# Kernel optimization log

Hardware: AMD Instinct MI355X
Metric: run time of the kernel (lower is better)

The kernel has to match this reference:

```python
import jax, jax.numpy as jnp
import numpy as np

R_TOKEN_MAX = 32
R_CHAIN_MAX = 2
C_PAIR = 128
D_TOK = 2 * R_TOKEN_MAX + 2   # 66, one-hot depth for pos / token offsets
D_CHAIN = 2 * R_CHAIN_MAX + 2 # 6, one-hot depth for chain offsets
D_IN = 2 * D_TOK + 1 + D_CHAIN  # 139, Linear in_features


def setup_inputs() -> dict:
    key = jax.random.key(0)
    ks = jax.random.split(key, 6)
    B, N = 1, 1024
    residue_index = jnp.sort(jax.random.randint(ks[0], (B, N), 0, 1200, dtype=jnp.int32), axis=-1)
    token_index = jnp.broadcast_to(jnp.arange(N, dtype=jnp.int32), (B, N))
    asym_id = jnp.sort(jax.random.randint(ks[1], (B, N), 0, 8, dtype=jnp.int32), axis=-1)
    entity_id = jnp.sort(jax.random.randint(ks[2], (B, N), 0, 4, dtype=jnp.int32), axis=-1)
    sym_id = jax.random.randint(ks[3], (B, N), 0, 8, dtype=jnp.int32)
    W = jax.random.normal(ks[4], (D_IN, C_PAIR), dtype=jnp.float32) * 0.02
    return {
        'residue_index': residue_index,
        'token_index': token_index,
        'asym_id': asym_id,
        'entity_id': entity_id,
        'sym_id': sym_id,
        'W': W,
    }


def _offset_index(fi, r_max, is_same):
    # offset[i, j] = fi[i] - fi[j]  (torch: unsqueeze(-1) - unsqueeze(-2))
    off = fi[..., :, None] - fi[..., None, :]
    clipped = jnp.clip(off + r_max, 0, 2 * r_max)
    # pairs not satisfying is_same go to the sentinel bucket 2*r_max + 1
    return jnp.where(is_same, clipped, 2 * r_max + 1)


def reference(residue_index, token_index, asym_id, entity_id, sym_id, W):
    same_chain = asym_id[..., :, None] == asym_id[..., None, :]
    same_residue = residue_index[..., :, None] == residue_index[..., None, :]
    same_entity = entity_id[..., :, None] == entity_id[..., None, :]

    idx_pos = _offset_index(residue_index, R_TOKEN_MAX, same_residue)
    idx_tok = _offset_index(token_index, R_TOKEN_MAX, same_residue & same_chain)
    idx_chain = _offset_index(sym_id, R_CHAIN_MAX, ~same_chain)

    # Bias-free Linear on concatenated one-hots == sum of gathered weight rows.
    Wp = W[:D_TOK]                    # rel_pos block
    Wt = W[D_TOK:2 * D_TOK]           # rel_token block
    w_ent = W[2 * D_TOK]              # same_entity column (single row)
    Wc = W[2 * D_TOK + 1:]            # rel_chain block

    out = (jnp.take(Wp, idx_pos, axis=0)
           + jnp.take(Wt, idx_tok, axis=0)
           + same_entity[..., None].astype(W.dtype) * w_ent
           + jnp.take(Wc, idx_chain, axis=0))
    return out  # [B, N, N, C_PAIR]
```

## Files before the change

kernel.cpp:

```cpp
#include <hip/hip_runtime.h>


#define C_PAIR 128
#define N_COMBO 152

typedef float f4 __attribute__((ext_vector_type(4)));

__device__ __forceinline__ int combo_id(int ri, int ai, int ei, int ti, int si,
                                        int rj, int aj, int ej, int tj, int sj) {
    const bool sr = (ri == rj);
    const bool sc = (ai == aj);
    const bool se = (ei == ej);
    int cid;
    if (sc) {
        if (sr) {
            int dt = ti - tj + 32;
            dt = dt < 0 ? 0 : (dt > 64 ? 64 : dt);
            cid = dt + (se ? 65 : 0);
        } else {
            cid = 130 + (se ? 1 : 0);
        }
    } else {
        int dc = si - sj + 2;
        dc = dc < 0 ? 0 : (dc > 4 ? 4 : dc);
        cid = 132 + dc + (sr ? 5 : 0) + (se ? 10 : 0);
    }
    return cid;
}

__global__ __launch_bounds__(128) void rpe_combine(const float* __restrict__ W,
                                                   float* __restrict__ T) {
    const int cid = blockIdx.x;
    const int c   = threadIdx.x;
    int idx_pos, idx_tok, idx_chain, se;
    if (cid < 130) {
        se = cid >= 65 ? 1 : 0;
        idx_pos = 32; idx_tok = cid - se * 65; idx_chain = 5;
    } else if (cid < 132) {
        se = cid - 130;
        idx_pos = 65; idx_tok = 65; idx_chain = 5;
    } else {
        int r = cid - 132;
        se = r >= 10 ? 1 : 0; r -= se * 10;
        const int sr = r >= 5 ? 1 : 0; r -= sr * 5;
        idx_pos = sr ? 32 : 65; idx_tok = 65; idx_chain = r;
    }
    const float p  = W[idx_pos * C_PAIR + c];
    const float t  = W[(66 + idx_tok) * C_PAIR + c];
    const float e  = W[132 * C_PAIR + c];
    const float ch = W[(133 + idx_chain) * C_PAIR + c];
    const float fe = se ? 1.0f : 0.0f;
    T[cid * C_PAIR + c] = ((p + t) + fe * e) + ch;
}

__global__ __launch_bounds__(256) void rpe_apply(
    const int* __restrict__ res, const int* __restrict__ tok,
    const int* __restrict__ asym, const int* __restrict__ ent,
    const int* __restrict__ sym, const float* __restrict__ T,
    float* __restrict__ out, int N, int blocks_per_row)
{
    const int bid = blockIdx.x;
    const int i   = bid / blocks_per_row;
    const int jb  = bid - i * blocks_per_row;
    const int t   = threadIdx.x;
    const int c4  = t & 31;
    const int j1  = jb * 16 + (t >> 5);
    const int j2  = j1 + 8;

    const int ri = res[i], ai = asym[i], ei = ent[i], ti = tok[i], si = sym[i];

    const int cid1 = combo_id(ri, ai, ei, ti, si, res[j1], asym[j1], ent[j1], tok[j1], sym[j1]);
    const int cid2 = combo_id(ri, ai, ei, ti, si, res[j2], asym[j2], ent[j2], tok[j2], sym[j2]);

    const f4 v1 = ((const f4*)(T + (size_t)cid1 * C_PAIR))[c4];
    const f4 v2 = ((const f4*)(T + (size_t)cid2 * C_PAIR))[c4];

    f4* o = (f4*)out;
    __builtin_nontemporal_store(v1, o + ((size_t)i * N + j1) * 32 + c4);
    __builtin_nontemporal_store(v2, o + ((size_t)i * N + j2) * 32 + c4);
}

__global__ __launch_bounds__(256) void rpe_direct(
    const int* __restrict__ res, const int* __restrict__ tok,
    const int* __restrict__ asym, const int* __restrict__ ent,
    const int* __restrict__ sym, const float* __restrict__ W,
    float* __restrict__ out, int N, int blocks_per_row)
{
    const int bid = blockIdx.x;
    const int i  = bid / blocks_per_row;
    const int jb = bid - i * blocks_per_row;
    const int t  = threadIdx.x;
    const int j  = jb * 8 + (t >> 5);
    const int c4 = t & 31;

    const int ri = res[i],  rj = res[j];
    const int ai = asym[i], aj = asym[j];
    const int ei = ent[i],  ej = ent[j];
    const int ti = tok[i],  tj = tok[j];
    const int si = sym[i],  sj = sym[j];

    const bool sr = (ri == rj);
    const bool sc = (ai == aj);
    const bool se = (ei == ej);

    const int idx_pos = sr ? 32 : 65;
    int dt = ti - tj + 32; dt = dt < 0 ? 0 : (dt > 64 ? 64 : dt);
    const int idx_tok = (sr && sc) ? dt : 65;
    int dc = si - sj + 2; dc = dc < 0 ? 0 : (dc > 4 ? 4 : dc);
    const int idx_chain = (!sc) ? dc : 5;

    const f4 p  = ((const f4*)(W + (size_t)idx_pos * C_PAIR))[c4];
    const f4 tk = ((const f4*)(W + (size_t)(66 + idx_tok) * C_PAIR))[c4];
    const f4 e  = ((const f4*)(W + (size_t)132 * C_PAIR))[c4];
    const f4 c  = ((const f4*)(W + (size_t)(133 + idx_chain) * C_PAIR))[c4];
    const float fe = se ? 1.0f : 0.0f;

    f4 r;
    r.x = ((p.x + tk.x) + fe * e.x) + c.x;
    r.y = ((p.y + tk.y) + fe * e.y) + c.y;
    r.z = ((p.z + tk.z) + fe * e.z) + c.z;
    r.w = ((p.w + tk.w) + fe * e.w) + c.w;

    ((f4*)(out + ((size_t)i * N + j) * C_PAIR))[c4] = r;
}

extern "C" void kernel_launch(void* const* d_in, const int* in_sizes, int n_in,
                              void* d_out, int out_size, void* d_ws, size_t ws_size,
                              hipStream_t stream) {
    const int* res  = (const int*)d_in[0];
    const int* tok  = (const int*)d_in[1];
    const int* asym = (const int*)d_in[2];
    const int* ent  = (const int*)d_in[3];
    const int* sym  = (const int*)d_in[4];
    const float* W  = (const float*)d_in[5];
    float* out = (float*)d_out;

    const int N = in_sizes[0];
    const size_t table_bytes = (size_t)N_COMBO * C_PAIR * sizeof(float);

    if (ws_size >= table_bytes && (N % 16) == 0) {
        float* T = (float*)d_ws;
        rpe_combine<<<N_COMBO, 128, 0, stream>>>(W, T);
        const int blocks_per_row = N / 16;
        rpe_apply<<<N * blocks_per_row, 256, 0, stream>>>(res, tok, asym, ent, sym,
                                                          T, out, N, blocks_per_row);
    } else {
        const int blocks_per_row = N / 8;
        rpe_direct<<<N * blocks_per_row, 256, 0, stream>>>(res, tok, asym, ent, sym,
                                                           W, out, N, blocks_per_row);
    }
}
```

Baseline: 101.6 us.

## Fuse combo-table build into per-row kernel with shared-memory table and cids

Replaces the two-kernel scheme (global combo table plus apply) with a single kernel of one block per output row. Each block rebuilds the full 152-entry combined weight table in LDS (about 78 KB) and precomputes the combo ids for all 1024 columns, then streams the row out from shared memory. This removes the second launch and the global table round trip. In exchange every block redoes the table build, the large LDS footprint limits occupancy, and the stores are no longer nontemporal.

```diff
diff --git a/kernel.cpp b/kernel.cpp
--- a/kernel.cpp
+++ b/kernel.cpp
@@ -3,6 +3,7 @@
 
 #define C_PAIR 128
 #define N_COMBO 152
+#define NTOK 1024
 
 typedef float f4 __attribute__((ext_vector_type(4)));
 
@@ -28,11 +29,8 @@
     return cid;
 }
 
-__global__ __launch_bounds__(128) void rpe_combine(const float* __restrict__ W,
-                                                   float* __restrict__ T) {
-    const int cid = blockIdx.x;
-    const int c   = threadIdx.x;
-    int idx_pos, idx_tok, idx_chain, se;
+__device__ __forceinline__ void decode_cid(int cid, int& idx_pos, int& idx_tok,
+                                           int& idx_chain, int& se) {
     if (cid < 130) {
         se = cid >= 65 ? 1 : 0;
         idx_pos = 32; idx_tok = cid - se * 65; idx_chain = 5;
@@ -45,39 +43,59 @@
         const int sr = r >= 5 ? 1 : 0; r -= sr * 5;
         idx_pos = sr ? 32 : 65; idx_tok = 65; idx_chain = r;
     }
-    const float p  = W[idx_pos * C_PAIR + c];
-    const float t  = W[(66 + idx_tok) * C_PAIR + c];
-    const float e  = W[132 * C_PAIR + c];
-    const float ch = W[(133 + idx_chain) * C_PAIR + c];
-    const float fe = se ? 1.0f : 0.0f;
-    T[cid * C_PAIR + c] = ((p + t) + fe * e) + ch;
 }
 
-__global__ __launch_bounds__(256) void rpe_apply(
+__global__ __launch_bounds__(256) void rpe_fused(
     const int* __restrict__ res, const int* __restrict__ tok,
     const int* __restrict__ asym, const int* __restrict__ ent,
-    const int* __restrict__ sym, const float* __restrict__ T,
-    float* __restrict__ out, int N, int blocks_per_row)
+    const int* __restrict__ sym, const float* __restrict__ W,
+    float* __restrict__ out)
 {
-    const int bid = blockIdx.x;
-    const int i   = bid / blocks_per_row;
-    const int jb  = bid - i * blocks_per_row;
-    const int t   = threadIdx.x;
-    const int c4  = t & 31;
-    const int j1  = jb * 16 + (t >> 5);
-    const int j2  = j1 + 8;
+    __shared__ f4 s_T[N_COMBO * 32];
+    __shared__ unsigned short s_cid[NTOK];
+
+    const int i = blockIdx.x;
+    const int t = threadIdx.x;
 
     const int ri = res[i], ai = asym[i], ei = ent[i], ti = tok[i], si = sym[i];
 
-    const int cid1 = combo_id(ri, ai, ei, ti, si, res[j1], asym[j1], ent[j1], tok[j1], sym[j1]);
-    const int cid2 = combo_id(ri, ai, ei, ti, si, res[j2], asym[j2], ent[j2], tok[j2], sym[j2]);
+    #pragma unroll
+    for (int k = 0; k < NTOK / 256; ++k) {
+        const int j = t + k * 256;
+        s_cid[j] = (unsigned short)combo_id(ri, ai, ei, ti, si,
+                       res[j], asym[j], ent[j], tok[j], sym[j]);
+    }
 
-    const f4 v1 = ((const f4*)(T + (size_t)cid1 * C_PAIR))[c4];
-    const f4 v2 = ((const f4*)(T + (size_t)cid2 * C_PAIR))[c4];
+    #pragma unroll
+    for (int k = 0; k < 19; ++k) {
+        const int idx = t + k * 256;
+        const int cid = idx >> 5;
+        const int ch  = idx & 31;
+        int ip, it, ic, se;
+        decode_cid(cid, ip, it, ic, se);
+        const f4 p  = ((const f4*)(W + (size_t)ip * C_PAIR))[ch];
+        const f4 tk = ((const f4*)(W + (size_t)(66 + it) * C_PAIR))[ch];
+        const f4 e  = ((const f4*)(W + (size_t)132 * C_PAIR))[ch];
+        const f4 c  = ((const f4*)(W + (size_t)(133 + ic) * C_PAIR))[ch];
+        const float fe = se ? 1.0f : 0.0f;
+        f4 r;
+        r.x = ((p.x + tk.x) + fe * e.x) + c.x;
+        r.y = ((p.y + tk.y) + fe * e.y) + c.y;
+        r.z = ((p.z + tk.z) + fe * e.z) + c.z;
+        r.w = ((p.w + tk.w) + fe * e.w) + c.w;
+        s_T[idx] = r;
+    }
+    __syncthreads();
 
-    f4* o = (f4*)out;
-    __builtin_nontemporal_store(v1, o + ((size_t)i * N + j1) * 32 + c4);
-    __builtin_nontemporal_store(v2, o + ((size_t)i * N + j2) * 32 + c4);
+    const int sub = t >> 5;
+    const int ch  = t & 31;
+    f4* o = (f4*)out + ((size_t)i * NTOK + sub) * 32 + ch;
+    #pragma unroll 8
+    for (int jb = 0; jb < NTOK / 8; ++jb) {
+        const int j = jb * 8 + sub;
+        const int cid = s_cid[j];
+        o[(size_t)jb * 256] = s_T[cid * 32 + ch];
+    }
 }
 
 __global__ __launch_bounds__(256) void rpe_direct(
@@ -136,14 +154,9 @@
     float* out = (float*)d_out;
 
     const int N = in_sizes[0];
-    const size_t table_bytes = (size_t)N_COMBO * C_PAIR * sizeof(float);
 
-    if (ws_size >= table_bytes && (N % 16) == 0) {
-        float* T = (float*)d_ws;
-        rpe_combine<<<N_COMBO, 128, 0, stream>>>(W, T);
-        const int blocks_per_row = N / 16;
-        rpe_apply<<<N * blocks_per_row, 256, 0, stream>>>(res, tok, asym, ent, sym,
-                                                          T, out, N, blocks_per_row);
+    if (N == NTOK) {
+        rpe_fused<<<NTOK, 256, 0, stream>>>(res, tok, asym, ent, sym, W, out);
     } else {
         const int blocks_per_row = N / 8;
         rpe_direct<<<N * blocks_per_row, 256, 0, stream>>>(res, tok, asym, ent, sym,
```

Result: no change. 102.8 us (+1.2%).

## Tile apply kernel into 4x64 pair blocks with shared-memory combo ids

Applied to the files above, without the earlier changes.

The apply kernel now has each block cover a 4-row by 64-column tile of pairs instead of 16 pairs. Each thread computes one combo id into shared memory, and the block then loops 32 times to stream table rows out with nontemporal stores. This cuts the block count and the redundant per-pair index loads, and lets each thread issue many stores. The path is specialised to N equal to 1024, and other sizes fall back to the direct kernel.

```diff
diff --git a/kernel.cpp b/kernel.cpp
--- a/kernel.cpp
+++ b/kernel.cpp
@@ -3,6 +3,9 @@
 
 #define C_PAIR 128
 #define N_COMBO 152
+#define NTOK 1024
+#define ISEG 4
+#define JSEG 64
 
 typedef float f4 __attribute__((ext_vector_type(4)));
 
@@ -53,31 +56,41 @@
     T[cid * C_PAIR + c] = ((p + t) + fe * e) + ch;
 }
 
-__global__ __launch_bounds__(256) void rpe_apply(
+__global__ __launch_bounds__(256) void rpe_apply4x64(
     const int* __restrict__ res, const int* __restrict__ tok,
     const int* __restrict__ asym, const int* __restrict__ ent,
     const int* __restrict__ sym, const float* __restrict__ T,
-    float* __restrict__ out, int N, int blocks_per_row)
+    float* __restrict__ out)
 {
-    const int bid = blockIdx.x;
-    const int i   = bid / blocks_per_row;
-    const int jb  = bid - i * blocks_per_row;
-    const int t   = threadIdx.x;
-    const int c4  = t & 31;
-    const int j1  = jb * 16 + (t >> 5);
-    const int j2  = j1 + 8;
+    __shared__ unsigned short s_cid[ISEG * JSEG];
 
-    const int ri = res[i], ai = asym[i], ei = ent[i], ti = tok[i], si = sym[i];
+    const int bid  = blockIdx.x;
+    const int nseg = NTOK / JSEG;
+    const int i0   = (bid / nseg) * ISEG;
+    const int j0   = (bid % nseg) * JSEG;
+    const int t    = threadIdx.x;
 
-    const int cid1 = combo_id(ri, ai, ei, ti, si, res[j1], asym[j1], ent[j1], tok[j1], sym[j1]);
-    const int cid2 = combo_id(ri, ai, ei, ti, si, res[j2], asym[j2], ent[j2], tok[j2], sym[j2]);
+    {
+        const int ii = t >> 6, jj = t & 63;
+        const int i = i0 + ii, j = j0 + jj;
+        s_cid[ii * JSEG + jj] = (unsigned short)combo_id(
+            res[i], asym[i], ent[i], tok[i], sym[i],
+            res[j], asym[j], ent[j], tok[j], sym[j]);
+    }
+    __syncthreads();
 
-    const f4 v1 = ((const f4*)(T + (size_t)cid1 * C_PAIR))[c4];
-    const f4 v2 = ((const f4*)(T + (size_t)cid2 * C_PAIR))[c4];
-
-    f4* o = (f4*)out;
-    __builtin_nontemporal_store(v1, o + ((size_t)i * N + j1) * 32 + c4);
-    __builtin_nontemporal_store(v2, o + ((size_t)i * N + j2) * 32 + c4);
+    const int sub = t >> 5;
+    const int ch  = t & 31;
+    #pragma unroll 8
+    for (int it = 0; it < 32; ++it) {
+        const int ii = it >> 3;
+        const int jb = it & 7;
+        const int j  = jb * 8 + sub;
+        const int cid = s_cid[ii * JSEG + j];
+        const f4 v = ((const f4*)(T + (size_t)cid * C_PAIR))[ch];
+        __builtin_nontemporal_store(
+            v, (f4*)out + (((size_t)(i0 + ii) * NTOK) + j0 + j) * 32 + ch);
+    }
 }
 
 __global__ __launch_bounds__(256) void rpe_direct(
@@ -138,12 +151,11 @@
     const int N = in_sizes[0];
     const size_t table_bytes = (size_t)N_COMBO * C_PAIR * sizeof(float);
 
-    if (ws_size >= table_bytes && (N % 16) == 0) {
+    if (N == NTOK && ws_size >= table_bytes) {
         float* T = (float*)d_ws;
         rpe_combine<<<N_COMBO, 128, 0, stream>>>(W, T);
-        const int blocks_per_row = N / 16;
-        rpe_apply<<<N * blocks_per_row, 256, 0, stream>>>(res, tok, asym, ent, sym,
-                                                          T, out, N, blocks_per_row);
+        const int grid = (NTOK / ISEG) * (NTOK / JSEG);
+        rpe_apply4x64<<<grid, 256, 0, stream>>>(res, tok, asym, ent, sym, T, out);
     } else {
         const int blocks_per_row = N / 8;
         rpe_direct<<<N * blocks_per_row, 256, 0, stream>>>(res, tok, asym, ent, sym,
```

Measured after the change: 107.5 us. +5.8%, slower.

## Use fixed-size grid with deep per-thread store batching and shuffled combo ids

Applied to the files above, without the earlier changes.

Replaces the one-block-per-16-columns launch with a fixed 2048-block grid where each block loops over 8 chunks of 64 columns. Combo ids are computed once per lane and broadcast via wave shuffles, and each thread issues 8 table loads then 8 nontemporal stores. This aims to cut block launch overhead and raise memory-level parallelism for the write-bound output, but hardcodes N=1024 and computes ids redundantly across waves.

```diff
diff --git a/kernel.cpp b/kernel.cpp
--- a/kernel.cpp
+++ b/kernel.cpp
@@ -3,6 +3,9 @@
 
 #define C_PAIR 128
 #define N_COMBO 152
+#define NTOK 1024
+#define NBLK 2048
+#define BTHR 256
 
 typedef float f4 __attribute__((ext_vector_type(4)));
 
@@ -53,31 +56,42 @@
     T[cid * C_PAIR + c] = ((p + t) + fe * e) + ch;
 }
 
-__global__ __launch_bounds__(256) void rpe_apply(
+__global__ __launch_bounds__(BTHR) void rpe_apply_deep(
     const int* __restrict__ res, const int* __restrict__ tok,
     const int* __restrict__ asym, const int* __restrict__ ent,
     const int* __restrict__ sym, const float* __restrict__ T,
-    float* __restrict__ out, int N, int blocks_per_row)
+    float* __restrict__ out)
 {
-    const int bid = blockIdx.x;
-    const int i   = bid / blocks_per_row;
-    const int jb  = bid - i * blocks_per_row;
-    const int t   = threadIdx.x;
-    const int c4  = t & 31;
-    const int j1  = jb * 16 + (t >> 5);
-    const int j2  = j1 + 8;
+    const int b = blockIdx.x;
+    const int t = threadIdx.x;
+    const int l = t & 63;
+    const int s = t >> 5;
+    const int c = t & 31;
 
-    const int ri = res[i], ai = asym[i], ei = ent[i], ti = tok[i], si = sym[i];
+    #pragma unroll
+    for (int k = 0; k < 8; ++k) {
+        const int chunk = k * NBLK + b;
+        const int i  = chunk >> 4;
+        const int j0 = (chunk & 15) << 6;
 
-    const int cid1 = combo_id(ri, ai, ei, ti, si, res[j1], asym[j1], ent[j1], tok[j1], sym[j1]);
-    const int cid2 = combo_id(ri, ai, ei, ti, si, res[j2], asym[j2], ent[j2], tok[j2], sym[j2]);
+        const int ri = res[i], ai = asym[i], ei = ent[i], ti = tok[i], si = sym[i];
+        const int j = j0 + l;
+        const int mycid = combo_id(ri, ai, ei, ti, si,
+                                   res[j], asym[j], ent[j], tok[j], sym[j]);
 
-    const f4 v1 = ((const f4*)(T + (size_t)cid1 * C_PAIR))[c4];
-    const f4 v2 = ((const f4*)(T + (size_t)cid2 * C_PAIR))[c4];
+        f4 vv[8];
+        #pragma unroll
+        for (int u = 0; u < 8; ++u) {
+            const int cid_u = __shfl(mycid, u * 8 + s, 64);
+            vv[u] = ((const f4*)(T + (size_t)cid_u * C_PAIR))[c];
+        }
 
-    f4* o = (f4*)out;
-    __builtin_nontemporal_store(v1, o + ((size_t)i * N + j1) * 32 + c4);
-    __builtin_nontemporal_store(v2, o + ((size_t)i * N + j2) * 32 + c4);
+        f4* o = (f4*)out + (size_t)chunk * 2048 + t;
+        #pragma unroll
+        for (int u = 0; u < 8; ++u) {
+            __builtin_nontemporal_store(vv[u], o + u * 256);
+        }
+    }
 }
 
 __global__ __launch_bounds__(256) void rpe_direct(
@@ -138,12 +152,10 @@
     const int N = in_sizes[0];
     const size_t table_bytes = (size_t)N_COMBO * C_PAIR * sizeof(float);
 
-    if (ws_size >= table_bytes && (N % 16) == 0) {
+    if (N == NTOK && ws_size >= table_bytes) {
         float* T = (float*)d_ws;
         rpe_combine<<<N_COMBO, 128, 0, stream>>>(W, T);
-        const int blocks_per_row = N / 16;
-        rpe_apply<<<N * blocks_per_row, 256, 0, stream>>>(res, tok, asym, ent, sym,
-                                                          T, out, N, blocks_per_row);
+        rpe_apply_deep<<<NBLK, BTHR, 0, stream>>>(res, tok, asym, ent, sym, T, out);
     } else {
         const int blocks_per_row = N / 8;
         rpe_direct<<<N * blocks_per_row, 256, 0, stream>>>(res, tok, asym, ent, sym,
```

Result: slower. 112.0 us (+10.2%).
